# Optimization experiments

Measured on AMD Instinct MI355X. Metric: run time of the kernel, lower is better.

## Reference

```python
import jax, jax.numpy as jnp
import numpy as np

B, S, HID = 2, 4096, 2048
NH, NKV, HD = 32, 8, 64
GROUPS = NH // NKV
ROPE_THETA = 10000.0


def _rope_cos_sin(seq_len, dim, dtype):
    inv_freq = 1.0 / (ROPE_THETA ** (jnp.arange(0, dim, 2, dtype=jnp.float32) / dim))
    pos = jnp.arange(seq_len, dtype=jnp.float32)
    freqs = pos[:, None] * inv_freq[None, :]          # [S, D/2]
    emb = jnp.concatenate([freqs, freqs], axis=-1)    # [S, D]
    return jnp.cos(emb).astype(dtype), jnp.sin(emb).astype(dtype)


def _rotate_half(x):
    x1, x2 = jnp.split(x, 2, axis=-1)
    return jnp.concatenate([-x2, x1], axis=-1)


def _apply_rope(x, cos, sin):
    # x: [B, H, S, D]; cos/sin: [S, D]
    return x * cos[None, None] + _rotate_half(x) * sin[None, None]


def kappa(x):
    return jax.nn.elu(x) + 1.0


def setup_inputs() -> dict:
    key = jax.random.key(0)
    ks = jax.random.split(key, 6)
    sc = 0.02
    return {
        "hidden_states": jax.random.normal(ks[0], (B, S, HID), jnp.float32),
        "Wq": jax.random.normal(ks[1], (HID, NH * HD), jnp.float32) * sc,
        "Wk": jax.random.normal(ks[2], (HID, NKV * HD), jnp.float32) * sc,
        "Wv": jax.random.normal(ks[3], (HID, NKV * HD), jnp.float32) * sc,
        "Wphi": jax.random.normal(ks[4], (HID, HID), jnp.float32) * sc,
        "Wo": jax.random.normal(ks[5], (HID, HID), jnp.float32) * sc,
    }


def reference(hidden_states, Wq, Wk, Wv, Wphi, Wo):
    bsz, q_len, _ = hidden_states.shape

    q = (hidden_states @ Wq).reshape(bsz, q_len, NH, HD).transpose(0, 2, 1, 3)   # [B,NH,S,D]
    k = (hidden_states @ Wk).reshape(bsz, q_len, NKV, HD).transpose(0, 2, 1, 3)  # [B,NKV,S,D]
    v = (hidden_states @ Wv).reshape(bsz, q_len, NKV, HD).transpose(0, 2, 1, 3)

    cos, sin = _rope_cos_sin(q_len, HD, hidden_states.dtype)
    q = _apply_rope(q, cos, sin)
    k = _apply_rope(k, cos, sin)

    # repeat_kv for GQA: [B,NKV,S,D] -> [B,NH,S,D]
    k = jnp.repeat(k, GROUPS, axis=1)
    v = jnp.repeat(v, GROUPS, axis=1)

    Qk = kappa(q)   # [B,NH,S,D]
    Kk = kappa(k)

    Qg = Qk.mean(axis=2)                                # [B,NH,D] global query
    logits = jnp.einsum("bnd,bnsd->bns", Qg, Kk)        # [B,NH,S]
    alpha = jax.nn.softmax(logits, axis=-1) * float(q_len)

    # KV aggregation: [B,NH,D,D] state
    outer_sum = jnp.einsum("bns,bnsd,bnsf->bndf", alpha, Kk, v)
    result_attn = jnp.einsum("bnsd,bndf->bnsf", Qk, outer_sum)  # [B,NH,S,D]

    X_phi = (hidden_states @ Wphi).reshape(bsz, q_len, NH, HD).transpose(0, 2, 1, 3)
    ctx = (X_phi * result_attn).transpose(0, 2, 1, 3).reshape(bsz, q_len, HID)
    return ctx @ Wo
```

## Files before the change

### kernel.cpp

```cpp
#include <hip/hip_runtime.h>
#include <hip/hip_bf16.h>

#define B_ 2
#define S_ 4096
#define HID_ 2048
#define NH_ 32
#define NKV_ 8
#define HD_ 64
#define GROUPS_ 4
#define NCH_ 32
#define NLIN_ 5120

typedef short short8 __attribute__((ext_vector_type(8)));
typedef float floatx4 __attribute__((ext_vector_type(4)));

__device__ __forceinline__ float bf2f(unsigned short u){
  union { unsigned int i; float f; } v; v.i = ((unsigned int)u) << 16; return v.f;
}
__device__ __forceinline__ unsigned short f2bf(float f){
  union { float f; unsigned int i; } v; v.f = f;
  unsigned int i = v.i;
  unsigned int r = (i + 0x7fffu + ((i >> 16) & 1u)) >> 16;
  return (unsigned short)r;
}

__device__ __forceinline__ void async_copy16(unsigned short* lds, const unsigned short* g){
  __builtin_amdgcn_global_load_lds((const __attribute__((address_space(1))) void*)g,
                                   (__attribute__((address_space(3))) void*)lds,
                                   16, 0, 0);
}

__global__ void conv_bf16(const float* __restrict__ x, unsigned short* __restrict__ y, int n4){
  int i = blockIdx.x * 256 + threadIdx.x;
  if (i < n4){
    float4 v = ((const float4*)x)[i];
    ushort4 o;
    o.x = f2bf(v.x); o.y = f2bf(v.y); o.z = f2bf(v.z); o.w = f2bf(v.w);
    ((ushort4*)y)[i] = o;
  }
}

__global__ void transpose_to_bf16(const float* __restrict__ W, unsigned short* __restrict__ Wt,
                                  int K, int N){
  __shared__ float tile[32][33];
  int n0 = blockIdx.x * 32, k0 = blockIdx.y * 32;
  int tx = threadIdx.x, ty = threadIdx.y;
  #pragma unroll
  for (int j = 0; j < 4; j++)
    tile[ty + j*8][tx] = W[(size_t)(k0 + ty + j*8) * N + n0 + tx];
  __syncthreads();
  #pragma unroll
  for (int j = 0; j < 4; j++)
    Wt[(size_t)(n0 + ty + j*8) * K + k0 + tx] = f2bf(tile[tx][ty + j*8]);
}

#define GTILE 16384

__global__ __launch_bounds__(512, 2) void gemm256(
    const unsigned short* __restrict__ A, const unsigned short* __restrict__ Bt,
    void* __restrict__ Cv, int M, int N, int K, int cbf16)
{
  __shared__ __align__(16) unsigned short As[2 * GTILE];
  __shared__ __align__(16) unsigned short Bs[2 * GTILE];

  const int tid = threadIdx.x;
  const int w = tid >> 6, lane = tid & 63;
  const int wr = w >> 2, wc = w & 3;
  const int l15 = lane & 15, quad = lane >> 4;

  const int nbx = N >> 8;
  int flat = blockIdx.y * nbx + blockIdx.x;
  int nwg  = nbx * (M >> 8);
  int cpx  = nwg >> 3;
  int swz  = (flat & 7) * cpx + (flat >> 3);
  int bx = swz % nbx, by = swz / nbx;
  const int m0 = by << 8, n0 = bx << 8;

  const int srow = (w << 3) + (lane >> 3);
  const int scc  = (lane & 7) ^ (lane >> 3);
  const unsigned short* gA = A  + (size_t)(m0 + srow) * K + scc * 8;
  const unsigned short* gB = Bt + (size_t)(n0 + srow) * K + scc * 8;
  const size_t rs64  = (size_t)64  * K;
  const size_t rs128 = (size_t)128 * K;
  unsigned short* lA0 = As + (w << 9);
  unsigned short* lB0 = Bs + (w << 9);

#define STAGE_A(bsel, h, t) do { \
    unsigned short* _d = lA0 + (bsel) * GTILE + (h) * 8192; \
    const unsigned short* _g = gA + (size_t)(h) * rs128 + (size_t)(t) * 64; \
    async_copy16(_d, _g); \
    async_copy16(_d + 4096, _g + rs64); \
  } while (0)
#define STAGE_B(bsel, h, t) do { \
    unsigned short* _d = lB0 + (bsel) * GTILE + (h) * 8192; \
    const unsigned short* _g = gB + (size_t)(h) * rs128 + (size_t)(t) * 64; \
    async_copy16(_d, _g); \
    async_copy16(_d + 4096, _g + rs64); \
  } while (0)
#define SCHED0 __builtin_amdgcn_sched_barrier(0)

  const int ks0  = ((quad     ^ (lane & 7)) << 3);
  const int ks1  = (((4+quad) ^ (lane & 7)) << 3);
  const int arow = (wr * 128 + l15) * 64;
  const int brow = (wc * 64  + l15) * 64;

  floatx4 acc[8][4] = {};
  short8 af[8][2], bfr[4][2];

  const int nt = K >> 6;

  STAGE_A(0, 0, 0); STAGE_A(0, 1, 0); STAGE_B(0, 0, 0); STAGE_B(0, 1, 0);
  if (nt > 1){
    STAGE_A(1, 0, 1); STAGE_A(1, 1, 1); STAGE_B(1, 0, 1); STAGE_B(1, 1, 1);
    asm volatile("s_waitcnt vmcnt(8)" ::: "memory");
  } else {
    asm volatile("s_waitcnt vmcnt(0)" ::: "memory");
  }
  SCHED0;
  __builtin_amdgcn_s_barrier();
  SCHED0;

  for (int T = 0; T < nt; ++T){
    const int cb = T & 1;
    const unsigned short* Ab = As + cb * GTILE;
    const unsigned short* Bb = Bs + cb * GTILE;

    #pragma unroll
    for (int m = 0; m < 4; ++m){
      af[m][0] = *(const short8*)(Ab + arow + m * 1024 + ks0);
      af[m][1] = *(const short8*)(Ab + arow + m * 1024 + ks1);
    }
    #pragma unroll
    for (int n = 0; n < 2; ++n){
      bfr[n][0] = *(const short8*)(Bb + brow + n * 1024 + ks0);
      bfr[n][1] = *(const short8*)(Bb + brow + n * 1024 + ks1);
    }
    SCHED0; __builtin_amdgcn_s_barrier(); SCHED0;
    __builtin_amdgcn_s_setprio(1);
    #pragma unroll
    for (int k = 0; k < 2; ++k)
      #pragma unroll
      for (int m = 0; m < 4; ++m)
        #pragma unroll
        for (int n = 0; n < 2; ++n)
          acc[m][n] = __builtin_amdgcn_mfma_f32_16x16x32_bf16(af[m][k], bfr[n][k], acc[m][n], 0, 0, 0);
    __builtin_amdgcn_s_setprio(0);
    SCHED0; __builtin_amdgcn_s_barrier(); SCHED0;

    #pragma unroll
    for (int m = 0; m < 4; ++m){
      af[4+m][0] = *(const short8*)(Ab + arow + (4+m) * 1024 + ks0);
      af[4+m][1] = *(const short8*)(Ab + arow + (4+m) * 1024 + ks1);
    }
    #pragma unroll
    for (int n = 0; n < 2; ++n){
      bfr[2+n][0] = *(const short8*)(Bb + brow + (2+n) * 1024 + ks0);
      bfr[2+n][1] = *(const short8*)(Bb + brow + (2+n) * 1024 + ks1);
    }
    SCHED0; __builtin_amdgcn_s_barrier(); SCHED0;
    __builtin_amdgcn_s_setprio(1);
    #pragma unroll
    for (int k = 0; k < 2; ++k)
      #pragma unroll
      for (int m = 0; m < 4; ++m)
        #pragma unroll
        for (int n = 0; n < 2; ++n)
          acc[m][2+n] = __builtin_amdgcn_mfma_f32_16x16x32_bf16(af[m][k], bfr[2+n][k], acc[m][2+n], 0, 0, 0);
    __builtin_amdgcn_s_setprio(0);
    SCHED0; __builtin_amdgcn_s_barrier(); SCHED0;

    if (T + 2 < nt){ STAGE_A(cb, 0, T + 2); STAGE_A(cb, 1, T + 2); }
    SCHED0; __builtin_amdgcn_s_barrier(); SCHED0;
    __builtin_amdgcn_s_setprio(1);
    #pragma unroll
    for (int k = 0; k < 2; ++k)
      #pragma unroll
      for (int m = 0; m < 4; ++m)
        #pragma unroll
        for (int n = 0; n < 2; ++n)
          acc[4+m][n] = __builtin_amdgcn_mfma_f32_16x16x32_bf16(af[4+m][k], bfr[n][k], acc[4+m][n], 0, 0, 0);
    __builtin_amdgcn_s_setprio(0);
    SCHED0; __builtin_amdgcn_s_barrier(); SCHED0;

    if (T + 2 < nt){
      STAGE_B(cb, 0, T + 2); STAGE_B(cb, 1, T + 2);
      asm volatile("s_waitcnt vmcnt(8)" ::: "memory");
    } else {
      asm volatile("s_waitcnt vmcnt(0)" ::: "memory");
    }
    SCHED0; __builtin_amdgcn_s_barrier(); SCHED0;
    __builtin_amdgcn_s_setprio(1);
    #pragma unroll
    for (int k = 0; k < 2; ++k)
      #pragma unroll
      for (int m = 0; m < 4; ++m)
        #pragma unroll
        for (int n = 0; n < 2; ++n)
          acc[4+m][2+n] = __builtin_amdgcn_mfma_f32_16x16x32_bf16(af[4+m][k], bfr[2+n][k], acc[4+m][2+n], 0, 0, 0);
    __builtin_amdgcn_s_setprio(0);
    SCHED0; __builtin_amdgcn_s_barrier(); SCHED0;
  }

#undef STAGE_A
#undef STAGE_B
#undef SCHED0

  if (cbf16){
    unsigned short* Cb = (unsigned short*)Cv;
    #pragma unroll
    for (int mi = 0; mi < 8; ++mi){
      const int row = m0 + wr * 128 + mi * 16 + quad * 4;
      #pragma unroll
      for (int ni = 0; ni < 4; ++ni){
        const int col = n0 + wc * 64 + ni * 16 + l15;
        #pragma unroll
        for (int r = 0; r < 4; ++r)
          Cb[(size_t)(row + r) * N + col] = f2bf(acc[mi][ni][r]);
      }
    }
  } else {
    float* Cf = (float*)Cv;
    #pragma unroll
    for (int mi = 0; mi < 8; ++mi){
      const int row = m0 + wr * 128 + mi * 16 + quad * 4;
      #pragma unroll
      for (int ni = 0; ni < 4; ++ni){
        const int col = n0 + wc * 64 + ni * 16 + l15;
        #pragma unroll
        for (int r = 0; r < 4; ++r)
          Cf[(size_t)(row + r) * N + col] = acc[mi][ni][r];
      }
    }
  }
}

__global__ void rope_kappa_q(const unsigned short* __restrict__ lin, unsigned short* __restrict__ Qk){
  int idx = blockIdx.x * 256 + threadIdx.x;
  int i = idx & 31;
  int n = (idx >> 5) & (NH_ - 1);
  int s = (idx >> 10) & (S_ - 1);
  int b = idx >> 22;
  float invf = exp2f(-(float)i * (13.287712379549449f / 32.0f));
  float ang = (float)s * invf;
  float c = cosf(ang), sn = sinf(ang);
  size_t in_o = (size_t)(b * S_ + s) * NLIN_ + n * HD_;
  float x1 = bf2f(lin[in_o + i]);
  float x2 = bf2f(lin[in_o + i + 32]);
  float r1 = x1 * c - x2 * sn;
  float r2 = x2 * c + x1 * sn;
  r1 = r1 > 0.f ? r1 + 1.f : __expf(r1);
  r2 = r2 > 0.f ? r2 + 1.f : __expf(r2);
  size_t o = ((size_t)(b * NH_ + n) * S_ + s) * HD_;
  Qk[o + i] = f2bf(r1);
  Qk[o + i + 32] = f2bf(r2);
}

__global__ void rope_kappa_k(const unsigned short* __restrict__ lin, unsigned short* __restrict__ Kk){
  int idx = blockIdx.x * 256 + threadIdx.x;
  int i = idx & 31;
  int kv = (idx >> 5) & (NKV_ - 1);
  int s = (idx >> 8) & (S_ - 1);
  int b = idx >> 20;
  float invf = exp2f(-(float)i * (13.287712379549449f / 32.0f));
  float ang = (float)s * invf;
  float c = cosf(ang), sn = sinf(ang);
  size_t in_o = (size_t)(b * S_ + s) * NLIN_ + 2048 + kv * HD_;
  float x1 = bf2f(lin[in_o + i]);
  float x2 = bf2f(lin[in_o + i + 32]);
  float r1 = x1 * c - x2 * sn;
  float r2 = x2 * c + x1 * sn;
  r1 = r1 > 0.f ? r1 + 1.f : __expf(r1);
  r2 = r2 > 0.f ? r2 + 1.f : __expf(r2);
  size_t o = ((size_t)(b * NKV_ + kv) * S_ + s) * HD_;
  Kk[o + i] = f2bf(r1);
  Kk[o + i + 32] = f2bf(r2);
}

__global__ __launch_bounds__(256) void qg_mean(const unsigned short* __restrict__ Qk,
                                               float* __restrict__ Qg){
  int bn = blockIdx.x, chunk = blockIdx.y;
  int tid = threadIdx.x;
  int dgrp = tid & 7, sgrp = tid >> 3;
  const unsigned short* base = Qk + (size_t)bn * S_ * HD_
                             + (size_t)(chunk * 256 + sgrp) * HD_ + dgrp * 8;
  float acc[8] = {};
  #pragma unroll
  for (int i = 0; i < 8; i++){
    short8 v = *(const short8*)(base + (size_t)i * 32 * HD_);
    #pragma unroll
    for (int e = 0; e < 8; e++) acc[e] += bf2f((unsigned short)v[e]);
  }
  __shared__ float red[256][8];
  #pragma unroll
  for (int e = 0; e < 8; e++) red[tid][e] = acc[e];
  __syncthreads();
  if (tid < 64){
    int dg = tid >> 3, e = tid & 7;
    float s = 0.f;
    #pragma unroll
    for (int g = 0; g < 32; g++) s += red[g * 8 + dg][e];
    atomicAdd(&Qg[bn * 64 + tid], s * (1.0f / (float)S_));
  }
}

__global__ __launch_bounds__(256) void logits_kernel(const unsigned short* __restrict__ Kk,
                                                     const float* __restrict__ Qg,
                                                     float* __restrict__ logits){
  int bn = blockIdx.x, chunk = blockIdx.y;
  int b = bn / NH_, n = bn % NH_, kv = n / GROUPS_;
  int tid = threadIdx.x;
  __shared__ float qg[64];
  if (tid < 64) qg[tid] = Qg[bn * 64 + tid];
  __syncthreads();
  int s = chunk * 256 + tid;
  const unsigned short* row = Kk + ((size_t)(b * NKV_ + kv) * S_ + s) * HD_;
  float acc = 0.f;
  #pragma unroll
  for (int c = 0; c < 8; c++){
    short8 v = *(const short8*)(row + c * 8);
    #pragma unroll
    for (int e = 0; e < 8; e++) acc += qg[c * 8 + e] * bf2f((unsigned short)v[e]);
  }
  logits[(size_t)bn * S_ + s] = acc;
}

__global__ __launch_bounds__(256) void softmax_kernel(const float* __restrict__ logits,
                                                      float* __restrict__ alpha){
  int bn = blockIdx.x;
  int tid = threadIdx.x;
  float l[16];
  float mymax = -1e30f;
  #pragma unroll
  for (int j = 0; j < 16; j++){
    l[j] = logits[(size_t)bn * S_ + j * 256 + tid];
    mymax = fmaxf(mymax, l[j]);
  }
  __shared__ float red[256];
  red[tid] = mymax; __syncthreads();
  for (int st = 128; st > 0; st >>= 1){
    if (tid < st) red[tid] = fmaxf(red[tid], red[tid + st]);
    __syncthreads();
  }
  float gmax = red[0];
  __syncthreads();
  float mysum = 0.f;
  #pragma unroll
  for (int j = 0; j < 16; j++){ l[j] = __expf(l[j] - gmax); mysum += l[j]; }
  red[tid] = mysum; __syncthreads();
  for (int st = 128; st > 0; st >>= 1){
    if (tid < st) red[tid] += red[tid + st];
    __syncthreads();
  }
  float inv = (float)S_ / red[0];
  #pragma unroll
  for (int j = 0; j < 16; j++)
    alpha[(size_t)bn * S_ + j * 256 + tid] = l[j] * inv;
}

__global__ __launch_bounds__(256) void outer_sum_kernel(const unsigned short* __restrict__ Kk,
                                                        const unsigned short* __restrict__ lin,
                                                        const float* __restrict__ alpha,
                                                        float* __restrict__ part){
  int bkv = blockIdx.x, chunk = blockIdx.y;
  int b = bkv >> 3, kv = bkv & 7;
  int tid = threadIdx.x;
  int d = tid >> 2, fb = (tid & 3) * 16;
  __shared__ float ks[64][64];
  __shared__ float vs[64][64];
  __shared__ float as[4][64];
  float acc[4][16] = {};
  const unsigned short* kb = Kk + (size_t)(b * NKV_ + kv) * S_ * HD_;
  const int SPC = S_ / NCH_;

  for (int t = 0; t < SPC / 64; t++){
    int ss = chunk * SPC + t * 64;
    #pragma unroll
    for (int jj = 0; jj < 4; jj++){
      int idx4 = jj * 256 + tid;
      int si = idx4 >> 4, c4 = (idx4 & 15) * 4;
      ushort4 kv4 = *(const ushort4*)(kb + (size_t)(ss + si) * HD_ + c4);
      ks[si][c4]   = bf2f(kv4.x); ks[si][c4+1] = bf2f(kv4.y);
      ks[si][c4+2] = bf2f(kv4.z); ks[si][c4+3] = bf2f(kv4.w);
      ushort4 vv4 = *(const ushort4*)(lin + (size_t)(b * S_ + ss + si) * NLIN_ + 2560 + kv * HD_ + c4);
      vs[si][c4]   = bf2f(vv4.x); vs[si][c4+1] = bf2f(vv4.y);
      vs[si][c4+2] = bf2f(vv4.z); vs[si][c4+3] = bf2f(vv4.w);
    }
    {
      int h = tid >> 6, si = tid & 63;
      as[h][si] = alpha[(size_t)(b * NH_ + kv * GROUPS_ + h) * S_ + ss + si];
    }
    __syncthreads();
    #pragma unroll 4
    for (int si = 0; si < 64; si++){
      float k = ks[si][d];
      float4 v0 = *(const float4*)&vs[si][fb];
      float4 v1 = *(const float4*)&vs[si][fb + 4];
      float4 v2 = *(const float4*)&vs[si][fb + 8];
      float4 v3 = *(const float4*)&vs[si][fb + 12];
      #pragma unroll
      for (int h = 0; h < 4; h++){
        float ak = as[h][si] * k;
        acc[h][0]  += ak * v0.x; acc[h][1]  += ak * v0.y; acc[h][2]  += ak * v0.z; acc[h][3]  += ak * v0.w;
        acc[h][4]  += ak * v1.x; acc[h][5]  += ak * v1.y; acc[h][6]  += ak * v1.z; acc[h][7]  += ak * v1.w;
        acc[h][8]  += ak * v2.x; acc[h][9]  += ak * v2.y; acc[h][10] += ak * v2.z; acc[h][11] += ak * v2.w;
        acc[h][12] += ak * v3.x; acc[h][13] += ak * v3.y; acc[h][14] += ak * v3.z; acc[h][15] += ak * v3.w;
      }
    }
    __syncthreads();
  }

  #pragma unroll
  for (int h = 0; h < 4; h++){
    float* pb = part + ((size_t)(chunk * 16 + bkv) * 4 + h) * 4096 + d * 64 + fb;
    #pragma unroll
    for (int j = 0; j < 4; j++)
      *(float4*)&pb[j * 4] = *(float4*)&acc[h][j * 4];
  }
}

__global__ __launch_bounds__(256) void osum_reduce_t(const float* __restrict__ part,
                                                     unsigned short* __restrict__ osumb){
  int bn = blockIdx.x;
  int tid = threadIdx.x;
  __shared__ float os[64][65];
  const float4* p4 = (const float4*)part;
  #pragma unroll
  for (int r = 0; r < 4; r++){
    int idx4 = r * 256 + tid;
    float4 s = {0.f, 0.f, 0.f, 0.f};
    #pragma unroll 8
    for (int c = 0; c < NCH_; c++){
      float4 v = p4[(size_t)c * 65536 + bn * 1024 + idx4];
      s.x += v.x; s.y += v.y; s.z += v.z; s.w += v.w;
    }
    int d = idx4 >> 4;
    int f0 = (idx4 & 15) * 4;
    os[d][f0] = s.x; os[d][f0+1] = s.y; os[d][f0+2] = s.z; os[d][f0+3] = s.w;
  }
  __syncthreads();
  int f = tid >> 2, d0 = (tid & 3) * 16;
  unsigned short hi[16], lo[16];
  #pragma unroll
  for (int j = 0; j < 16; j++){
    float x = os[d0 + j][f];
    unsigned short h = f2bf(x);
    hi[j] = h;
    lo[j] = f2bf(x - bf2f(h));
  }
  unsigned short* oh = osumb + ((size_t)bn * 2) * 4096 + (size_t)f * 64 + d0;
  unsigned short* ol = oh + 4096;
  *(short8*)(oh)     = *(const short8*)(hi);
  *(short8*)(oh + 8) = *(const short8*)(hi + 8);
  *(short8*)(ol)     = *(const short8*)(lo);
  *(short8*)(ol + 8) = *(const short8*)(lo + 8);
}

__global__ __launch_bounds__(256) void ctx_mfma(const unsigned short* __restrict__ Qk,
                                                const unsigned short* __restrict__ osumb,
                                                const unsigned short* __restrict__ lin,
                                                unsigned short* __restrict__ ctx){
  int bn = blockIdx.x, sc = blockIdx.y;
  int b = bn >> 5, n = bn & 31;
  int tid = threadIdx.x;
  int w = tid >> 6, lane = tid & 63;
  int l15 = lane & 15, quad = lane >> 4;

  const unsigned short* obase = osumb + ((size_t)bn * 2) * 4096;
  short8 bh[4][2], bl[4][2];
  #pragma unroll
  for (int nf = 0; nf < 4; nf++){
    int f = nf * 16 + l15;
    #pragma unroll
    for (int kh = 0; kh < 2; kh++){
      bh[nf][kh] = *(const short8*)(obase + (size_t)f * 64 + kh * 32 + quad * 8);
      bl[nf][kh] = *(const short8*)(obase + 4096 + (size_t)f * 64 + kh * 32 + quad * 8);
    }
  }

  int s0 = sc * 256 + w * 64;
  const unsigned short* qbase = Qk + ((size_t)bn * S_ + s0) * HD_;
  floatx4 acc[4][4] = {};
  #pragma unroll
  for (int m = 0; m < 4; m++){
    short8 a0 = *(const short8*)(qbase + (size_t)(m * 16 + l15) * HD_ + quad * 8);
    short8 a1 = *(const short8*)(qbase + (size_t)(m * 16 + l15) * HD_ + 32 + quad * 8);
    #pragma unroll
    for (int nf = 0; nf < 4; nf++){
      acc[m][nf] = __builtin_amdgcn_mfma_f32_16x16x32_bf16(a0, bh[nf][0], acc[m][nf], 0, 0, 0);
      acc[m][nf] = __builtin_amdgcn_mfma_f32_16x16x32_bf16(a1, bh[nf][1], acc[m][nf], 0, 0, 0);
      acc[m][nf] = __builtin_amdgcn_mfma_f32_16x16x32_bf16(a0, bl[nf][0], acc[m][nf], 0, 0, 0);
      acc[m][nf] = __builtin_amdgcn_mfma_f32_16x16x32_bf16(a1, bl[nf][1], acc[m][nf], 0, 0, 0);
    }
  }

  #pragma unroll
  for (int m = 0; m < 4; m++){
    #pragma unroll
    for (int r = 0; r < 4; r++){
      int s = s0 + m * 16 + quad * 4 + r;
      const unsigned short* xp = lin + (size_t)(b * S_ + s) * NLIN_ + 3072 + n * HD_;
      unsigned short* cp = ctx + (size_t)(b * S_ + s) * HID_ + n * HD_;
      #pragma unroll
      for (int nf = 0; nf < 4; nf++){
        int f = nf * 16 + l15;
        cp[f] = f2bf(bf2f(xp[f]) * acc[m][nf][r]);
      }
    }
  }
}

extern "C" void kernel_launch(void* const* d_in, const int* in_sizes, int n_in,
                              void* d_out, int out_size, void* d_ws, size_t ws_size,
                              hipStream_t stream) {
  const float* hs   = (const float*)d_in[0];
  const float* Wq   = (const float*)d_in[1];
  const float* Wk   = (const float*)d_in[2];
  const float* Wv   = (const float*)d_in[3];
  const float* Wphi = (const float*)d_in[4];
  const float* Wo   = (const float*)d_in[5];
  float* out = (float*)d_out;

  char* ws = (char*)d_ws;
  const size_t M = (size_t)B_ * S_;
  size_t off = 0;
  auto alloc = [&](size_t bytes){ size_t o = off; off += (bytes + 255) & ~(size_t)255; return o; };

  size_t off_x     = alloc(M * HID_ * 4);
  size_t off_wcat  = alloc((size_t)NLIN_ * HID_ * 2);
  size_t off_wot   = alloc((size_t)HID_ * HID_ * 2);
  size_t off_lin   = alloc(M * NLIN_ * 2);
  size_t off_qk    = alloc(M * HID_ * 2);
  size_t off_kk    = alloc(M * 512 * 2);
  size_t off_qg    = alloc(64 * 64 * 4);
  size_t off_alph  = alloc((size_t)B_ * NH_ * S_ * 4);
  size_t off_osumb = alloc((size_t)64 * 2 * 4096 * 2);
  (void)ws_size;

  unsigned short* hsb  = (unsigned short*)(ws + off_x);
  float*          part = (float*)(ws + off_x);
  unsigned short* ctx  = (unsigned short*)(ws + off_x);
  unsigned short* wcat = (unsigned short*)(ws + off_wcat);
  unsigned short* wot  = (unsigned short*)(ws + off_wot);
  unsigned short* lin  = (unsigned short*)(ws + off_lin);
  unsigned short* qk = (unsigned short*)(ws + off_qk);
  unsigned short* kk = (unsigned short*)(ws + off_kk);
  float* qg   = (float*)(ws + off_qg);
  float* alph = (float*)(ws + off_alph);
  unsigned short* osumb = (unsigned short*)(ws + off_osumb);

  conv_bf16<<<(int)(M * HID_ / 4 / 256), 256, 0, stream>>>(hs, hsb, (int)(M * HID_ / 4));
  transpose_to_bf16<<<dim3(HID_/32, HID_/32), dim3(32,8), 0, stream>>>(Wq,   wcat,                          HID_, HID_);
  transpose_to_bf16<<<dim3(512/32,  HID_/32), dim3(32,8), 0, stream>>>(Wk,   wcat + (size_t)2048 * HID_,    HID_, 512);
  transpose_to_bf16<<<dim3(512/32,  HID_/32), dim3(32,8), 0, stream>>>(Wv,   wcat + (size_t)2560 * HID_,    HID_, 512);
  transpose_to_bf16<<<dim3(HID_/32, HID_/32), dim3(32,8), 0, stream>>>(Wphi, wcat + (size_t)3072 * HID_,    HID_, HID_);
  transpose_to_bf16<<<dim3(HID_/32, HID_/32), dim3(32,8), 0, stream>>>(Wo,   wot,                           HID_, HID_);
  gemm256<<<dim3(NLIN_/256, M/256), 512, 0, stream>>>(hsb, wcat, lin, (int)M, NLIN_, HID_, 1);
  rope_kappa_q<<<(int)(M * NH_ * 32 / 256), 256, 0, stream>>>(lin, qk);
  rope_kappa_k<<<(int)(M * NKV_ * 32 / 256), 256, 0, stream>>>(lin, kk);
  hipMemsetAsync(qg, 0, 64 * 64 * 4, stream);
  qg_mean<<<dim3(B_ * NH_, S_ / 256), 256, 0, stream>>>(qk, qg);
  logits_kernel<<<dim3(B_ * NH_, S_ / 256), 256, 0, stream>>>(kk, qg, alph);
  softmax_kernel<<<B_ * NH_, 256, 0, stream>>>(alph, alph);
  outer_sum_kernel<<<dim3(B_ * NKV_, NCH_), 256, 0, stream>>>(kk, lin, alph, part);
  osum_reduce_t<<<64, 256, 0, stream>>>(part, osumb);
  ctx_mfma<<<dim3(B_ * NH_, S_ / 64 / 4), 256, 0, stream>>>(qk, osumb, lin, ctx);
  gemm256<<<dim3(HID_/256, M/256), 512, 0, stream>>>(ctx, wot, out, (int)M, HID_, HID_, 0);
}
```

Before: 545.0 us.

## Merge weight transposes and rope launches, restructure GEMM main loop, vectorize alpha loads

Folds the five weight transpose launches into one 3D-grid launch and the two rope/kappa launches into one, removing per-launch overhead. The GEMM inner loop is cut from four compute phases to two, loading all A/B fragments up front and issuing the prefetch of both tiles together, which means fewer barriers but more live registers. The outer-sum kernel stores alpha as [s][h] so one float4 LDS read replaces four scalar reads. Holding all fragments at once may push register pressure up, and the coarser schedule hides less load latency behind MFMAs.

Result: no change. 538.8 us (-1.1%).

```diff
diff --git a/kernel.cpp b/kernel.cpp
--- a/kernel.cpp
+++ b/kernel.cpp
@@ -40,10 +40,21 @@
   }
 }
 
-__global__ void transpose_to_bf16(const float* __restrict__ W, unsigned short* __restrict__ Wt,
-                                  int K, int N){
+__global__ void transpose_all(const float* __restrict__ Wq, const float* __restrict__ Wk,
+                              const float* __restrict__ Wv, const float* __restrict__ Wphi,
+                              const float* __restrict__ Wo,
+                              unsigned short* __restrict__ wcat, unsigned short* __restrict__ wot){
+  const float* W; unsigned short* Wt; int N;
+  switch (blockIdx.z){
+    case 0:  W = Wq;   Wt = wcat;                              N = 2048; break;
+    case 1:  W = Wk;   Wt = wcat + (size_t)2048 * HID_;        N = 512;  break;
+    case 2:  W = Wv;   Wt = wcat + (size_t)2560 * HID_;        N = 512;  break;
+    case 3:  W = Wphi; Wt = wcat + (size_t)3072 * HID_;        N = 2048; break;
+    default: W = Wo;   Wt = wot;                               N = 2048; break;
+  }
+  int n0 = blockIdx.x * 32, k0 = blockIdx.y * 32;
+  if (n0 >= N) return;
   __shared__ float tile[32][33];
-  int n0 = blockIdx.x * 32, k0 = blockIdx.y * 32;
   int tx = threadIdx.x, ty = threadIdx.y;
   #pragma unroll
   for (int j = 0; j < 4; j++)
@@ -51,7 +62,7 @@
   __syncthreads();
   #pragma unroll
   for (int j = 0; j < 4; j++)
-    Wt[(size_t)(n0 + ty + j*8) * K + k0 + tx] = f2bf(tile[tx][ty + j*8]);
+    Wt[(size_t)(n0 + ty + j*8) * HID_ + k0 + tx] = f2bf(tile[tx][ty + j*8]);
 }
 
 #define GTILE 16384
@@ -126,12 +137,12 @@
     const unsigned short* Bb = Bs + cb * GTILE;
 
     #pragma unroll
-    for (int m = 0; m < 4; ++m){
+    for (int m = 0; m < 8; ++m){
       af[m][0] = *(const short8*)(Ab + arow + m * 1024 + ks0);
       af[m][1] = *(const short8*)(Ab + arow + m * 1024 + ks1);
     }
     #pragma unroll
-    for (int n = 0; n < 2; ++n){
+    for (int n = 0; n < 4; ++n){
       bfr[n][0] = *(const short8*)(Bb + brow + n * 1024 + ks0);
       bfr[n][1] = *(const short8*)(Bb + brow + n * 1024 + ks1);
     }
@@ -142,20 +153,17 @@
       #pragma unroll
       for (int m = 0; m < 4; ++m)
         #pragma unroll
-        for (int n = 0; n < 2; ++n)
+        for (int n = 0; n < 4; ++n)
           acc[m][n] = __builtin_amdgcn_mfma_f32_16x16x32_bf16(af[m][k], bfr[n][k], acc[m][n], 0, 0, 0);
     __builtin_amdgcn_s_setprio(0);
     SCHED0; __builtin_amdgcn_s_barrier(); SCHED0;
 
-    #pragma unroll
-    for (int m = 0; m < 4; ++m){
-      af[4+m][0] = *(const short8*)(Ab + arow + (4+m) * 1024 + ks0);
-      af[4+m][1] = *(const short8*)(Ab + arow + (4+m) * 1024 + ks1);
-    }
-    #pragma unroll
-    for (int n = 0; n < 2; ++n){
-      bfr[2+n][0] = *(const short8*)(Bb + brow + (2+n) * 1024 + ks0);
-      bfr[2+n][1] = *(const short8*)(Bb + brow + (2+n) * 1024 + ks1);
+    if (T + 2 < nt){
+      STAGE_A(cb, 0, T + 2); STAGE_A(cb, 1, T + 2);
+      STAGE_B(cb, 0, T + 2); STAGE_B(cb, 1, T + 2);
+      asm volatile("s_waitcnt vmcnt(8)" ::: "memory");
+    } else {
+      asm volatile("s_waitcnt vmcnt(0)" ::: "memory");
     }
     SCHED0; __builtin_amdgcn_s_barrier(); SCHED0;
     __builtin_amdgcn_s_setprio(1);
@@ -164,39 +172,8 @@
       #pragma unroll
       for (int m = 0; m < 4; ++m)
         #pragma unroll
-        for (int n = 0; n < 2; ++n)
-          acc[m][2+n] = __builtin_amdgcn_mfma_f32_16x16x32_bf16(af[m][k], bfr[2+n][k], acc[m][2+n], 0, 0, 0);
-    __builtin_amdgcn_s_setprio(0);
-    SCHED0; __builtin_amdgcn_s_barrier(); SCHED0;
-
-    if (T + 2 < nt){ STAGE_A(cb, 0, T + 2); STAGE_A(cb, 1, T + 2); }
-    SCHED0; __builtin_amdgcn_s_barrier(); SCHED0;
-    __builtin_amdgcn_s_setprio(1);
-    #pragma unroll
-    for (int k = 0; k < 2; ++k)
-      #pragma unroll
-      for (int m = 0; m < 4; ++m)
-        #pragma unroll
-        for (int n = 0; n < 2; ++n)
+        for (int n = 0; n < 4; ++n)
           acc[4+m][n] = __builtin_amdgcn_mfma_f32_16x16x32_bf16(af[4+m][k], bfr[n][k], acc[4+m][n], 0, 0, 0);
-    __builtin_amdgcn_s_setprio(0);
-    SCHED0; __builtin_amdgcn_s_barrier(); SCHED0;
-
-    if (T + 2 < nt){
-      STAGE_B(cb, 0, T + 2); STAGE_B(cb, 1, T + 2);
-      asm volatile("s_waitcnt vmcnt(8)" ::: "memory");
-    } else {
-      asm volatile("s_waitcnt vmcnt(0)" ::: "memory");
-    }
-    SCHED0; __builtin_amdgcn_s_barrier(); SCHED0;
-    __builtin_amdgcn_s_setprio(1);
-    #pragma unroll
-    for (int k = 0; k < 2; ++k)
-      #pragma unroll
-      for (int m = 0; m < 4; ++m)
-        #pragma unroll
-        for (int n = 0; n < 2; ++n)
-          acc[4+m][2+n] = __builtin_amdgcn_mfma_f32_16x16x32_bf16(af[4+m][k], bfr[2+n][k], acc[4+m][2+n], 0, 0, 0);
     __builtin_amdgcn_s_setprio(0);
     SCHED0; __builtin_amdgcn_s_barrier(); SCHED0;
   }
@@ -234,46 +211,48 @@
   }
 }
 
-__global__ void rope_kappa_q(const unsigned short* __restrict__ lin, unsigned short* __restrict__ Qk){
-  int idx = blockIdx.x * 256 + threadIdx.x;
-  int i = idx & 31;
-  int n = (idx >> 5) & (NH_ - 1);
-  int s = (idx >> 10) & (S_ - 1);
-  int b = idx >> 22;
-  float invf = exp2f(-(float)i * (13.287712379549449f / 32.0f));
-  float ang = (float)s * invf;
-  float c = cosf(ang), sn = sinf(ang);
-  size_t in_o = (size_t)(b * S_ + s) * NLIN_ + n * HD_;
-  float x1 = bf2f(lin[in_o + i]);
-  float x2 = bf2f(lin[in_o + i + 32]);
-  float r1 = x1 * c - x2 * sn;
-  float r2 = x2 * c + x1 * sn;
-  r1 = r1 > 0.f ? r1 + 1.f : __expf(r1);
-  r2 = r2 > 0.f ? r2 + 1.f : __expf(r2);
-  size_t o = ((size_t)(b * NH_ + n) * S_ + s) * HD_;
-  Qk[o + i] = f2bf(r1);
-  Qk[o + i + 32] = f2bf(r2);
-}
-
-__global__ void rope_kappa_k(const unsigned short* __restrict__ lin, unsigned short* __restrict__ Kk){
-  int idx = blockIdx.x * 256 + threadIdx.x;
-  int i = idx & 31;
-  int kv = (idx >> 5) & (NKV_ - 1);
-  int s = (idx >> 8) & (S_ - 1);
-  int b = idx >> 20;
-  float invf = exp2f(-(float)i * (13.287712379549449f / 32.0f));
-  float ang = (float)s * invf;
-  float c = cosf(ang), sn = sinf(ang);
-  size_t in_o = (size_t)(b * S_ + s) * NLIN_ + 2048 + kv * HD_;
-  float x1 = bf2f(lin[in_o + i]);
-  float x2 = bf2f(lin[in_o + i + 32]);
-  float r1 = x1 * c - x2 * sn;
-  float r2 = x2 * c + x1 * sn;
-  r1 = r1 > 0.f ? r1 + 1.f : __expf(r1);
-  r2 = r2 > 0.f ? r2 + 1.f : __expf(r2);
-  size_t o = ((size_t)(b * NKV_ + kv) * S_ + s) * HD_;
-  Kk[o + i] = f2bf(r1);
-  Kk[o + i + 32] = f2bf(r2);
+__global__ void rope_fused(const unsigned short* __restrict__ lin,
+                           unsigned short* __restrict__ Qk, unsigned short* __restrict__ Kk){
+  int blk = blockIdx.x;
+  if (blk < 32768){
+    int idx = blk * 256 + threadIdx.x;
+    int i = idx & 31;
+    int n = (idx >> 5) & (NH_ - 1);
+    int s = (idx >> 10) & (S_ - 1);
+    int b = idx >> 22;
+    float invf = exp2f(-(float)i * (13.287712379549449f / 32.0f));
+    float ang = (float)s * invf;
+    float c = cosf(ang), sn = sinf(ang);
+    size_t in_o = (size_t)(b * S_ + s) * NLIN_ + n * HD_;
+    float x1 = bf2f(lin[in_o + i]);
+    float x2 = bf2f(lin[in_o + i + 32]);
+    float r1 = x1 * c - x2 * sn;
+    float r2 = x2 * c + x1 * sn;
+    r1 = r1 > 0.f ? r1 + 1.f : __expf(r1);
+    r2 = r2 > 0.f ? r2 + 1.f : __expf(r2);
+    size_t o = ((size_t)(b * NH_ + n) * S_ + s) * HD_;
+    Qk[o + i] = f2bf(r1);
+    Qk[o + i + 32] = f2bf(r2);
+  } else {
+    int idx = (blk - 32768) * 256 + threadIdx.x;
+    int i = idx & 31;
+    int kv = (idx >> 5) & (NKV_ - 1);
+    int s = (idx >> 8) & (S_ - 1);
+    int b = idx >> 20;
+    float invf = exp2f(-(float)i * (13.287712379549449f / 32.0f));
+    float ang = (float)s * invf;
+    float c = cosf(ang), sn = sinf(ang);
+    size_t in_o = (size_t)(b * S_ + s) * NLIN_ + 2048 + kv * HD_;
+    float x1 = bf2f(lin[in_o + i]);
+    float x2 = bf2f(lin[in_o + i + 32]);
+    float r1 = x1 * c - x2 * sn;
+    float r2 = x2 * c + x1 * sn;
+    r1 = r1 > 0.f ? r1 + 1.f : __expf(r1);
+    r2 = r2 > 0.f ? r2 + 1.f : __expf(r2);
+    size_t o = ((size_t)(b * NKV_ + kv) * S_ + s) * HD_;
+    Kk[o + i] = f2bf(r1);
+    Kk[o + i + 32] = f2bf(r2);
+  }
 }
 
 __global__ __launch_bounds__(256) void qg_mean(const unsigned short* __restrict__ Qk,
@@ -367,7 +346,7 @@
   int d = tid >> 2, fb = (tid & 3) * 16;
   __shared__ float ks[64][64];
   __shared__ float vs[64][64];
-  __shared__ float as[4][64];
+  __shared__ float as4[64][4];
   float acc[4][16] = {};
   const unsigned short* kb = Kk + (size_t)(b * NKV_ + kv) * S_ * HD_;
   const int SPC = S_ / NCH_;
@@ -386,25 +365,35 @@
       vs[si][c4+2] = bf2f(vv4.z); vs[si][c4+3] = bf2f(vv4.w);
     }
     {
-      int h = tid >> 6, si = tid & 63;
-      as[h][si] = alpha[(size_t)(b * NH_ + kv * GROUPS_ + h) * S_ + ss + si];
+      int si = tid >> 2, h = tid & 3;
+      as4[si][h] = alpha[(size_t)(b * NH_ + kv * GROUPS_ + h) * S_ + ss + si];
     }
     __syncthreads();
     #pragma unroll 4
     for (int si = 0; si < 64; si++){
       float k = ks[si][d];
+      float4 a4 = *(const float4*)&as4[si][0];
       float4 v0 = *(const float4*)&vs[si][fb];
       float4 v1 = *(const float4*)&vs[si][fb + 4];
       float4 v2 = *(const float4*)&vs[si][fb + 8];
       float4 v3 = *(const float4*)&vs[si][fb + 12];
-      #pragma unroll
-      for (int h = 0; h < 4; h++){
-        float ak = as[h][si] * k;
-        acc[h][0]  += ak * v0.x; acc[h][1]  += ak * v0.y; acc[h][2]  += ak * v0.z; acc[h][3]  += ak * v0.w;
-        acc[h][4]  += ak * v1.x; acc[h][5]  += ak * v1.y; acc[h][6]  += ak * v1.z; acc[h][7]  += ak * v1.w;
-        acc[h][8]  += ak * v2.x; acc[h][9]  += ak * v2.y; acc[h][10] += ak * v2.z; acc[h][11] += ak * v2.w;
-        acc[h][12] += ak * v3.x; acc[h][13] += ak * v3.y; acc[h][14] += ak * v3.z; acc[h][15] += ak * v3.w;
-      }
+      float ak0 = a4.x * k, ak1 = a4.y * k, ak2 = a4.z * k, ak3 = a4.w * k;
+      acc[0][0]  += ak0 * v0.x; acc[0][1]  += ak0 * v0.y; acc[0][2]  += ak0 * v0.z; acc[0][3]  += ak0 * v0.w;
+      acc[0][4]  += ak0 * v1.x; acc[0][5]  += ak0 * v1.y; acc[0][6]  += ak0 * v1.z; acc[0][7]  += ak0 * v1.w;
+      acc[0][8]  += ak0 * v2.x; acc[0][9]  += ak0 * v2.y; acc[0][10] += ak0 * v2.z; acc[0][11] += ak0 * v2.w;
+      acc[0][12] += ak0 * v3.x; acc[0][13] += ak0 * v3.y; acc[0][14] += ak0 * v3.z; acc[0][15] += ak0 * v3.w;
+      acc[1][0]  += ak1 * v0.x; acc[1][1]  += ak1 * v0.y; acc[1][2]  += ak1 * v0.z; acc[1][3]  += ak1 * v0.w;
+      acc[1][4]  += ak1 * v1.x; acc[1][5]  += ak1 * v1.y; acc[1][6]  += ak1 * v1.z; acc[1][7]  += ak1 * v1.w;
+      acc[1][8]  += ak1 * v2.x; acc[1][9]  += ak1 * v2.y; acc[1][10] += ak1 * v2.z; acc[1][11] += ak1 * v2.w;
+      acc[1][12] += ak1 * v3.x; acc[1][13] += ak1 * v3.y; acc[1][14] += ak1 * v3.z; acc[1][15] += ak1 * v3.w;
+      acc[2][0]  += ak2 * v0.x; acc[2][1]  += ak2 * v0.y; acc[2][2]  += ak2 * v0.z; acc[2][3]  += ak2 * v0.w;
+      acc[2][4]  += ak2 * v1.x; acc[2][5]  += ak2 * v1.y; acc[2][6]  += ak2 * v1.z; acc[2][7]  += ak2 * v1.w;
+      acc[2][8]  += ak2 * v2.x; acc[2][9]  += ak2 * v2.y; acc[2][10] += ak2 * v2.z; acc[2][11] += ak2 * v2.w;
+      acc[2][12] += ak2 * v3.x; acc[2][13] += ak2 * v3.y; acc[2][14] += ak2 * v3.z; acc[2][15] += ak2 * v3.w;
+      acc[3][0]  += ak3 * v0.x; acc[3][1]  += ak3 * v0.y; acc[3][2]  += ak3 * v0.z; acc[3][3]  += ak3 * v0.w;
+      acc[3][4]  += ak3 * v1.x; acc[3][5]  += ak3 * v1.y; acc[3][6]  += ak3 * v1.z; acc[3][7]  += ak3 * v1.w;
+      acc[3][8]  += ak3 * v2.x; acc[3][9]  += ak3 * v2.y; acc[3][10] += ak3 * v2.z; acc[3][11] += ak3 * v2.w;
+      acc[3][12] += ak3 * v3.x; acc[3][13] += ak3 * v3.y; acc[3][14] += ak3 * v3.z; acc[3][15] += ak3 * v3.w;
     }
     __syncthreads();
   }
@@ -549,14 +538,9 @@
   unsigned short* osumb = (unsigned short*)(ws + off_osumb);
 
   conv_bf16<<<(int)(M * HID_ / 4 / 256), 256, 0, stream>>>(hs, hsb, (int)(M * HID_ / 4));
-  transpose_to_bf16<<<dim3(HID_/32, HID_/32), dim3(32,8), 0, stream>>>(Wq,   wcat,                          HID_, HID_);
-  transpose_to_bf16<<<dim3(512/32,  HID_/32), dim3(32,8), 0, stream>>>(Wk,   wcat + (size_t)2048 * HID_,    HID_, 512);
-  transpose_to_bf16<<<dim3(512/32,  HID_/32), dim3(32,8), 0, stream>>>(Wv,   wcat + (size_t)2560 * HID_,    HID_, 512);
-  transpose_to_bf16<<<dim3(HID_/32, HID_/32), dim3(32,8), 0, stream>>>(Wphi, wcat + (size_t)3072 * HID_,    HID_, HID_);
-  transpose_to_bf16<<<dim3(HID_/32, HID_/32), dim3(32,8), 0, stream>>>(Wo,   wot,                           HID_, HID_);
+  transpose_all<<<dim3(64, 64, 5), dim3(32, 8), 0, stream>>>(Wq, Wk, Wv, Wphi, Wo, wcat, wot);
   gemm256<<<dim3(NLIN_/256, M/256), 512, 0, stream>>>(hsb, wcat, lin, (int)M, NLIN_, HID_, 1);
-  rope_kappa_q<<<(int)(M * NH_ * 32 / 256), 256, 0, stream>>>(lin, qk);
-  rope_kappa_k<<<(int)(M * NKV_ * 32 / 256), 256, 0, stream>>>(lin, kk);
+  rope_fused<<<32768 + 8192, 256, 0, stream>>>(lin, qk, kk);
   hipMemsetAsync(qg, 0, 64 * 64 * 4, stream);
   qg_mean<<<dim3(B_ * NH_, S_ / 256), 256, 0, stream>>>(qk, qg);
   logits_kernel<<<dim3(B_ * NH_, S_ / 256), 256, 0, stream>>>(kk, qg, alph);
```
